# Kernel tuning notes

Measured on AMD Instinct MI355X. Metric: run time of the kernel, lower is better.

## Reference

```python
import jax, jax.numpy as jnp
import numpy as np
from jax import lax

B, CIN, COUT, H, W = 4, 256, 256, 64, 64
KH = KW = 3
K = KH * KW
GN_GROUPS = 32
EPS = 1e-5


def setup_inputs() -> dict:
    key = jax.random.key(0)
    ks = jax.random.split(key, 6)
    x = jax.random.normal(ks[0], (B, CIN, H, W), jnp.float32)
    # offset predictor conv: 3x3, 18 out channels, with bias (init small so offsets stay near 0)
    offset_w = jax.random.normal(ks[1], (2 * K, CIN, KH, KW), jnp.float32) * 0.01
    offset_b = jax.random.normal(ks[2], (2 * K,), jnp.float32) * 0.01
    # deformable conv weight (no bias), He-ish scale
    deform_w = jax.random.normal(ks[3], (COUT, CIN, KH, KW), jnp.float32) * (1.0 / np.sqrt(CIN * K))
    gn_gamma = jnp.ones((COUT,), jnp.float32)
    gn_beta = jnp.zeros((COUT,), jnp.float32)
    return {"x": x, "offset_w": offset_w, "offset_b": offset_b,
            "deform_w": deform_w, "gn_gamma": gn_gamma, "gn_beta": gn_beta}


def _deform_conv(x, offset, weight):
    """Deformable conv v1, stride=1, pad=1, dil=1, deformable_groups=1.
    x: [B,C,H,W]; offset: [B,2K,H,W] with (dy,dx) per kernel tap; weight: [O,C,3,3].
    """
    b, c, h, w = x.shape
    off = offset.reshape(b, K, 2, h, w)
    # base sampling grid per kernel tap: p = p0 - pad + k
    ky, kx = jnp.meshgrid(jnp.arange(KH), jnp.arange(KW), indexing="ij")
    base_y = (jnp.arange(h, dtype=jnp.float32) - 1.0)[None, :, None] + ky.reshape(K).astype(jnp.float32)[:, None, None]  # [K,H,1]
    base_x = (jnp.arange(w, dtype=jnp.float32) - 1.0)[None, None, :] + kx.reshape(K).astype(jnp.float32)[:, None, None]  # [K,1,W]
    py = base_y[None] + off[:, :, 0]  # [B,K,H,W]
    px = base_x[None] + off[:, :, 1]  # [B,K,H,W]

    y0 = jnp.floor(py)
    x0 = jnp.floor(px)
    ty = py - y0
    tx = px - x0
    y0 = y0.astype(jnp.int32)
    x0 = x0.astype(jnp.int32)

    x_hw = x.transpose(0, 2, 3, 1).reshape(b, h * w, c)  # [B,HW,C]

    def corner(yi, xi, wgt):
        valid = (yi >= 0) & (yi < h) & (xi >= 0) & (xi < w)
        yc = jnp.clip(yi, 0, h - 1)
        xc = jnp.clip(xi, 0, w - 1)
        idx = (yc * w + xc).reshape(b, K * h * w)
        v = jnp.take_along_axis(x_hw, idx[..., None], axis=1)  # [B,KHW,C]
        return v * (wgt * valid.astype(wgt.dtype)).reshape(b, K * h * w, 1)

    samp = (corner(y0, x0, (1 - ty) * (1 - tx))
            + corner(y0, x0 + 1, (1 - ty) * tx)
            + corner(y0 + 1, x0, ty * (1 - tx))
            + corner(y0 + 1, x0 + 1, ty * tx))  # [B,KHW,C]
    samp = samp.reshape(b, K, h, w, c)
    return jnp.einsum("bkhwc,ock->bohw", samp, weight.reshape(weight.shape[0], c, K))


def reference(x, offset_w, offset_b, deform_w, gn_gamma, gn_beta):
    # offset = conv3x3(x) + bias
    offset = lax.conv_general_dilated(
        x, offset_w, window_strides=(1, 1), padding=((1, 1), (1, 1)),
        dimension_numbers=("NCHW", "OIHW", "NCHW")) + offset_b[None, :, None, None]
    out = _deform_conv(x, offset, deform_w)
    # GroupNorm(32, COUT) + ReLU
    b, c, h, w = out.shape
    g = out.reshape(b, GN_GROUPS, (c // GN_GROUPS) * h * w)
    mu = g.mean(axis=2, keepdims=True)
    var = g.var(axis=2, keepdims=True)
    g = (g - mu) * lax.rsqrt(var + EPS)
    out = g.reshape(b, c, h, w) * gn_gamma[None, :, None, None] + gn_beta[None, :, None, None]
    return jax.nn.relu(out)
```

## Files before the change

### kernel.cpp

```cpp
#include <hip/hip_runtime.h>
#include <hip/hip_bf16.h>
#include <stdint.h>


typedef unsigned short u16;
typedef __bf16 bf16x8 __attribute__((ext_vector_type(8)));
typedef float f32x4_t __attribute__((ext_vector_type(4)));

#define HW 4096

__device__ __forceinline__ uint32_t f32_to_bf16_rne(float f) {
  uint32_t u = __builtin_bit_cast(uint32_t, f);
  return (u + 0x7FFFu + ((u >> 16) & 1u)) >> 16;
}
__device__ __forceinline__ float bf_lo(uint32_t u) {
  return __builtin_bit_cast(float, u << 16);
}
__device__ __forceinline__ float bf_hi(uint32_t u) {
  return __builtin_bit_cast(float, u & 0xFFFF0000u);
}

__global__ __launch_bounds__(256) void k_transpose(const float* __restrict__ x,
                                                   u16* __restrict__ xt) {
  __shared__ float tile[32][33];
  int b = blockIdx.z;
  int c0 = blockIdx.y * 32;
  int p0 = blockIdx.x * 32;
  int tx = threadIdx.x, ty = threadIdx.y;
#pragma unroll
  for (int j = 0; j < 32; j += 8)
    tile[ty + j][tx] = x[(b * 256 + c0 + ty + j) * HW + p0 + tx];
  __syncthreads();
  int wid = ty * 32 + tx;
  int cp = wid & 15;
  int pr = wid >> 4;
#pragma unroll
  for (int j = 0; j < 2; j++) {
    int p = pr + j * 16;
    uint32_t lo = f32_to_bf16_rne(tile[cp * 2][p]);
    uint32_t hi = f32_to_bf16_rne(tile[cp * 2 + 1][p]);
    *(uint32_t*)&xt[(b * HW + p0 + p) * 256 + c0 + cp * 2] = lo | (hi << 16);
  }
}

__global__ __launch_bounds__(256) void k_prep_w(const float* __restrict__ wsrc,
                                                u16* __restrict__ warr) {
  int e = blockIdx.x * 256 + threadIdx.x;
  int kk = e & 7, m = (e >> 3) & 255, g = (e >> 11) & 7, kc = e >> 14;
  int cin = (kc & 3) * 64 + g * 8 + kk;
  int tap = kc >> 2;
  float v = wsrc[m * 2304 + cin * 9 + tap];
  warr[e] = (u16)f32_to_bf16_rne(v);
}

__global__ __launch_bounds__(256) void k_prep_owm(const float* __restrict__ ow,
                                                  u16* __restrict__ owm) {
  int e = blockIdx.x * 256 + threadIdx.x;
  int kk = e & 7, m = (e >> 3) & 31, g = (e >> 8) & 7, kc = e >> 11;
  int cin = (kc & 3) * 64 + g * 8 + kk;
  int tap = kc >> 2;
  float v = (m < 18) ? ow[m * 2304 + cin * 9 + tap] : 0.f;
  owm[e] = (u16)f32_to_bf16_rne(v);
}

__global__ __launch_bounds__(256) void k_conv(
    const u16* __restrict__ xt, const u16* __restrict__ warr,
    const u16* __restrict__ owm, const float* __restrict__ ob,
    float* __restrict__ out) {
  __shared__ char smem[27136];
  u16* stage = (u16*)smem;
  float* off_part = (float*)(smem + 16896);
  int4* ci_s = (int4*)smem;
  float4* mw_s = (float4*)(smem + 4608);
  u16* b_s = (u16*)(smem + 16896);

  int tid = threadIdx.x;
  int lane = tid & 63;
  int wm = tid >> 6;
  int b = blockIdx.x >> 7;
  int pt = blockIdx.x & 127;
  int p0 = pt * 32;
  int yrow = p0 >> 6, xbase = p0 & 63;

  {
    u16* st = stage + wm * 2112;
    int q = lane & 15, pq = lane >> 4;
    f32x4_t a2[2][2] = {};
#pragma unroll 1
    for (int tap = wm; tap < 9; tap += 4) {
      int ky = tap / 3, kx = tap % 3;
      int yy = yrow + ky - 1;
      bool vy = (yy >= 0) && (yy < 64);
#pragma unroll
      for (int cc = 0; cc < 4; cc++) {
        int kc = tap * 4 + cc;
#pragma unroll
        for (int i = 0; i < 8; i++) {
          int px = i * 4 + pq;
          int xx2 = xbase + px + kx - 1;
          uint2 v = make_uint2(0u, 0u);
          if (vy && xx2 >= 0 && xx2 < 64)
            v = *(const uint2*)&xt[(b * HW + yy * 64 + xx2) * 256 + cc * 64 + q * 4];
          *(uint2*)&st[(q >> 1) * 264 + px * 8 + (q & 1) * 4] = v;
        }
#pragma unroll
        for (int ks = 0; ks < 2; ks++) {
          int g = ks * 4 + pq;
          const u16* ab = owm + kc * 2048 + g * 256;
#pragma unroll
          for (int s = 0; s < 2; s++) {
            bf16x8 bfr = *(bf16x8*)&st[g * 264 + (s * 16 + q) * 8];
#pragma unroll
            for (int im = 0; im < 2; im++) {
              bf16x8 af = *(const bf16x8*)&ab[(im * 16 + q) * 8];
              a2[s][im] = __builtin_amdgcn_mfma_f32_16x16x32_bf16(af, bfr, a2[s][im], 0, 0, 0);
            }
          }
        }
      }
    }
#pragma unroll
    for (int s = 0; s < 2; s++)
#pragma unroll
      for (int im = 0; im < 2; im++)
#pragma unroll
        for (int r = 0; r < 4; r++) {
          int oc = im * 16 + pq * 4 + r;
          if (oc < 18) off_part[(wm * 32 + s * 16 + q) * 20 + oc] = a2[s][im][r];
        }
  }
  __syncthreads();
  for (int it = tid; it < 288; it += 256) {
    int tap = it >> 5;
    int px = it & 31;
    float dy = ob[2 * tap], dx = ob[2 * tap + 1];
#pragma unroll
    for (int wv = 0; wv < 4; wv++) {
      dy += off_part[(wv * 32 + px) * 20 + 2 * tap];
      dx += off_part[(wv * 32 + px) * 20 + 2 * tap + 1];
    }
    int ky = tap / 3, kx = tap % 3;
    int p = p0 + px;
    int yq = p >> 6, xq = p & 63;
    float py = (float)(yq - 1 + ky) + dy;
    float pxx = (float)(xq - 1 + kx) + dx;
    float y0f = floorf(py), x0f = floorf(pxx);
    float ty = py - y0f, tx = pxx - x0f;
    int y0 = (int)y0f, x0 = (int)x0f;
    int y1 = y0 + 1, x1 = x0 + 1;
    float wy0 = 1.f - ty, wy1 = ty, wx0 = 1.f - tx, wx1 = tx;
    bool vy0 = (y0 >= 0) && (y0 < 64), vy1 = (y1 >= 0) && (y1 < 64);
    bool vx0 = (x0 >= 0) && (x0 < 64), vx1 = (x1 >= 0) && (x1 < 64);
    int cy0 = min(max(y0, 0), 63), cy1 = min(max(y1, 0), 63);
    int cx0 = min(max(x0, 0), 63), cx1 = min(max(x1, 0), 63);
    int base = b * HW;
    int4 ci;
    ci.x = (base + cy0 * 64 + cx0) * 256;
    ci.y = (base + cy0 * 64 + cx1) * 256;
    ci.z = (base + cy1 * 64 + cx0) * 256;
    ci.w = (base + cy1 * 64 + cx1) * 256;
    float4 mw;
    mw.x = wy0 * wx0 * ((vy0 && vx0) ? 1.f : 0.f);
    mw.y = wy0 * wx1 * ((vy0 && vx1) ? 1.f : 0.f);
    mw.z = wy1 * wx0 * ((vy1 && vx0) ? 1.f : 0.f);
    mw.w = wy1 * wx1 * ((vy1 && vx1) ? 1.f : 0.f);
    ci_s[it] = ci;
    mw_s[it] = mw;
  }
  __syncthreads();

  int q = tid & 15, pxb = (tid >> 4) & 15;
  f32x4_t acc[2][4] = {};
#pragma unroll 1
  for (int tap = 0; tap < 9; tap++) {
    int4 ci0 = ci_s[tap * 32 + pxb];
    int4 ci1 = ci_s[tap * 32 + 16 + pxb];
    float4 mw0 = mw_s[tap * 32 + pxb];
    float4 mw1 = mw_s[tap * 32 + 16 + pxb];
#pragma unroll
    for (int cc = 0; cc < 4; cc++) {
      int kc = tap * 4 + cc;
      int e = cc * 64 + q * 4;
      u16* bb = b_s + (kc & 1) * 2176;
      {
        uint2 c0v = *(const uint2*)&xt[ci0.x + e];
        uint2 c1v = *(const uint2*)&xt[ci0.y + e];
        uint2 c2v = *(const uint2*)&xt[ci0.z + e];
        uint2 c3v = *(const uint2*)&xt[ci0.w + e];
        float r0 = mw0.x * bf_lo(c0v.x) + mw0.y * bf_lo(c1v.x) + mw0.z * bf_lo(c2v.x) + mw0.w * bf_lo(c3v.x);
        float r1 = mw0.x * bf_hi(c0v.x) + mw0.y * bf_hi(c1v.x) + mw0.z * bf_hi(c2v.x) + mw0.w * bf_hi(c3v.x);
        float r2 = mw0.x * bf_lo(c0v.y) + mw0.y * bf_lo(c1v.y) + mw0.z * bf_lo(c2v.y) + mw0.w * bf_lo(c3v.y);
        float r3 = mw0.x * bf_hi(c0v.y) + mw0.y * bf_hi(c1v.y) + mw0.z * bf_hi(c2v.y) + mw0.w * bf_hi(c3v.y);
        uint2 u;
        u.x = f32_to_bf16_rne(r0) | (f32_to_bf16_rne(r1) << 16);
        u.y = f32_to_bf16_rne(r2) | (f32_to_bf16_rne(r3) << 16);
        *(uint2*)&bb[(q >> 1) * 136 + pxb * 8 + (q & 1) * 4] = u;
      }
      {
        uint2 c0v = *(const uint2*)&xt[ci1.x + e];
        uint2 c1v = *(const uint2*)&xt[ci1.y + e];
        uint2 c2v = *(const uint2*)&xt[ci1.z + e];
        uint2 c3v = *(const uint2*)&xt[ci1.w + e];
        float r0 = mw1.x * bf_lo(c0v.x) + mw1.y * bf_lo(c1v.x) + mw1.z * bf_lo(c2v.x) + mw1.w * bf_lo(c3v.x);
        float r1 = mw1.x * bf_hi(c0v.x) + mw1.y * bf_hi(c1v.x) + mw1.z * bf_hi(c2v.x) + mw1.w * bf_hi(c3v.x);
        float r2 = mw1.x * bf_lo(c0v.y) + mw1.y * bf_lo(c1v.y) + mw1.z * bf_lo(c2v.y) + mw1.w * bf_lo(c3v.y);
        float r3 = mw1.x * bf_hi(c0v.y) + mw1.y * bf_hi(c1v.y) + mw1.z * bf_hi(c2v.y) + mw1.w * bf_hi(c3v.y);
        uint2 u;
        u.x = f32_to_bf16_rne(r0) | (f32_to_bf16_rne(r1) << 16);
        u.y = f32_to_bf16_rne(r2) | (f32_to_bf16_rne(r3) << 16);
        *(uint2*)&bb[1088 + (q >> 1) * 136 + pxb * 8 + (q & 1) * 4] = u;
      }
      __syncthreads();
#pragma unroll
      for (int ks = 0; ks < 2; ks++) {
        int g = ks * 4 + (lane >> 4);
        bf16x8 b0 = *(bf16x8*)&bb[g * 136 + (lane & 15) * 8];
        bf16x8 b1 = *(bf16x8*)&bb[1088 + g * 136 + (lane & 15) * 8];
        const u16* ab = warr + kc * 16384 + g * 2048 + (wm * 64 + (lane & 15)) * 8;
#pragma unroll
        for (int im = 0; im < 4; im++) {
          bf16x8 af = *(const bf16x8*)&ab[im * 128];
          acc[0][im] = __builtin_amdgcn_mfma_f32_16x16x32_bf16(af, b0, acc[0][im], 0, 0, 0);
          acc[1][im] = __builtin_amdgcn_mfma_f32_16x16x32_bf16(af, b1, acc[1][im], 0, 0, 0);
        }
      }
    }
  }
  int rq = lane >> 4;
#pragma unroll
  for (int s = 0; s < 2; s++) {
    int n = p0 + s * 16 + (lane & 15);
#pragma unroll
    for (int im = 0; im < 4; im++)
#pragma unroll
      for (int r = 0; r < 4; r++) {
        int m = wm * 64 + im * 16 + rq * 4 + r;
        out[(b * 256 + m) * HW + n] = acc[s][im][r];
      }
  }
}

__global__ __launch_bounds__(256) void k_gn_part(const float* __restrict__ out,
                                                 float2* __restrict__ part) {
  int blk = blockIdx.x;
  int bg = blk >> 2, qt = blk & 3;
  const float4* base = (const float4*)(out + (size_t)bg * 32768 + (size_t)qt * 8192);
  int tid = threadIdx.x;
  float s = 0.f, ss = 0.f;
#pragma unroll
  for (int i = 0; i < 8; i++) {
    float4 v = base[tid + i * 256];
    s += v.x + v.y + v.z + v.w;
    ss += v.x * v.x + v.y * v.y + v.z * v.z + v.w * v.w;
  }
#pragma unroll
  for (int m = 1; m < 64; m <<= 1) {
    s += __shfl_xor(s, m);
    ss += __shfl_xor(ss, m);
  }
  __shared__ float ls[4], lss[4];
  int wv = tid >> 6, lane = tid & 63;
  if (lane == 0) { ls[wv] = s; lss[wv] = ss; }
  __syncthreads();
  if (tid == 0)
    part[blk] = make_float2(ls[0] + ls[1] + ls[2] + ls[3],
                            lss[0] + lss[1] + lss[2] + lss[3]);
}

__global__ __launch_bounds__(256) void k_gn_apply(float* __restrict__ out,
                                                  const float2* __restrict__ part,
                                                  const float* __restrict__ gamma,
                                                  const float* __restrict__ beta) {
  __shared__ float sga, sbe;
  int gid = blockIdx.x * 256 + threadIdx.x;
  int c = (gid >> 10) & 255;
  int bb = gid >> 18;
  if (threadIdx.x == 0) {
    int p4 = (bb * 32 + (c >> 3)) * 4;
    float s = 0.f, ss = 0.f;
#pragma unroll
    for (int j = 0; j < 4; j++) {
      float2 p = part[p4 + j];
      s += p.x;
      ss += p.y;
    }
    float mu = s / 32768.f;
    float var = ss / 32768.f - mu * mu;
    float rs = rsqrtf(var + 1e-5f);
    float ga = gamma[c] * rs;
    sga = ga;
    sbe = beta[c] - mu * ga;
  }
  __syncthreads();
  float ga = sga, be = sbe;
  float4 v = ((const float4*)out)[gid];
  v.x = fmaxf(v.x * ga + be, 0.f);
  v.y = fmaxf(v.y * ga + be, 0.f);
  v.z = fmaxf(v.z * ga + be, 0.f);
  v.w = fmaxf(v.w * ga + be, 0.f);
  ((float4*)out)[gid] = v;
}

extern "C" void kernel_launch(void* const* d_in, const int* in_sizes, int n_in,
                              void* d_out, int out_size, void* d_ws, size_t ws_size,
                              hipStream_t stream) {
  const float* x = (const float*)d_in[0];
  const float* offset_w = (const float*)d_in[1];
  const float* offset_b = (const float*)d_in[2];
  const float* deform_w = (const float*)d_in[3];
  const float* gn_gamma = (const float*)d_in[4];
  const float* gn_beta = (const float*)d_in[5];
  float* out = (float*)d_out;
  char* ws = (char*)d_ws;

  u16* xt = (u16*)ws;
  u16* warr = (u16*)(ws + 8388608);
  u16* owm = (u16*)(ws + 9568256);
  float2* part = (float2*)(ws + 9715712);

  k_transpose<<<dim3(128, 8, 4), dim3(32, 8), 0, stream>>>(x, xt);
  k_prep_w<<<dim3(2304), dim3(256), 0, stream>>>(deform_w, warr);
  k_prep_owm<<<dim3(288), dim3(256), 0, stream>>>(offset_w, owm);
  k_conv<<<dim3(512), dim3(256), 0, stream>>>(xt, warr, owm, offset_b, out);
  k_gn_part<<<dim3(512), dim3(256), 0, stream>>>(out, part);
  k_gn_apply<<<dim3(4096), dim3(256), 0, stream>>>(out, part, gn_gamma, gn_beta);
}
```

Measured before the change: 173.6 us.

## Fuse GN stats into deform conv, widen to 512 threads, merge prep kernels

Merges the two weight-prep kernels into one launch that also zeroes the GroupNorm partial buffer. The deformable conv kernel moves to 512 threads with 8 waves, each owning 32 output channels. It uses 16-byte gathers, prefetches the next chunk's bilinear corner loads before the MFMA work, and processes 128 channels per barrier instead of 64. GroupNorm sum and sum-of-squares are now reduced in the conv epilogue and accumulated with atomics, which removes the separate stats pass over the output, at the cost of atomic contention and more LDS per block.

Result: faster. 163.4 us (-5.9%).

```diff
diff --git a/kernel.cpp b/kernel.cpp
--- a/kernel.cpp
+++ b/kernel.cpp
@@ -18,6 +18,12 @@
 }
 __device__ __forceinline__ float bf_hi(uint32_t u) {
   return __builtin_bit_cast(float, u & 0xFFFF0000u);
+}
+__device__ __forceinline__ uint32_t blend2(uint32_t a, uint32_t b, uint32_t c,
+                                           uint32_t d, float4 mw) {
+  float lo = mw.x * bf_lo(a) + mw.y * bf_lo(b) + mw.z * bf_lo(c) + mw.w * bf_lo(d);
+  float hi = mw.x * bf_hi(a) + mw.y * bf_hi(b) + mw.z * bf_hi(c) + mw.w * bf_hi(d);
+  return f32_to_bf16_rne(lo) | (f32_to_bf16_rne(hi) << 16);
 }
 
 __global__ __launch_bounds__(256) void k_transpose(const float* __restrict__ x,
@@ -43,36 +49,40 @@
   }
 }
 
-__global__ __launch_bounds__(256) void k_prep_w(const float* __restrict__ wsrc,
-                                                u16* __restrict__ warr) {
-  int e = blockIdx.x * 256 + threadIdx.x;
-  int kk = e & 7, m = (e >> 3) & 255, g = (e >> 11) & 7, kc = e >> 14;
-  int cin = (kc & 3) * 64 + g * 8 + kk;
-  int tap = kc >> 2;
-  float v = wsrc[m * 2304 + cin * 9 + tap];
-  warr[e] = (u16)f32_to_bf16_rne(v);
-}
-
-__global__ __launch_bounds__(256) void k_prep_owm(const float* __restrict__ ow,
-                                                  u16* __restrict__ owm) {
-  int e = blockIdx.x * 256 + threadIdx.x;
-  int kk = e & 7, m = (e >> 3) & 31, g = (e >> 8) & 7, kc = e >> 11;
-  int cin = (kc & 3) * 64 + g * 8 + kk;
-  int tap = kc >> 2;
-  float v = (m < 18) ? ow[m * 2304 + cin * 9 + tap] : 0.f;
-  owm[e] = (u16)f32_to_bf16_rne(v);
-}
-
-__global__ __launch_bounds__(256) void k_conv(
+__global__ __launch_bounds__(256) void k_prep(const float* __restrict__ wsrc,
+                                              const float* __restrict__ ow,
+                                              u16* __restrict__ warr,
+                                              u16* __restrict__ owm,
+                                              float* __restrict__ part) {
+  int bid = blockIdx.x;
+  if (bid < 2304) {
+    int e = bid * 256 + threadIdx.x;
+    int kk = e & 7, m = (e >> 3) & 255, g = (e >> 11) & 7, kc = e >> 14;
+    int cin = (kc & 3) * 64 + g * 8 + kk;
+    int tap = kc >> 2;
+    warr[e] = (u16)f32_to_bf16_rne(wsrc[m * 2304 + cin * 9 + tap]);
+  } else if (bid < 2592) {
+    int e = (bid - 2304) * 256 + threadIdx.x;
+    int kk = e & 7, m = (e >> 3) & 31, g = (e >> 8) & 7, kc = e >> 11;
+    int cin = (kc & 3) * 64 + g * 8 + kk;
+    int tap = kc >> 2;
+    float v = (m < 18) ? ow[m * 2304 + cin * 9 + tap] : 0.f;
+    owm[e] = (u16)f32_to_bf16_rne(v);
+  } else {
+    part[threadIdx.x] = 0.f;
+  }
+}
+
+__global__ __launch_bounds__(512, 4) void k_conv(
     const u16* __restrict__ xt, const u16* __restrict__ warr,
     const u16* __restrict__ owm, const float* __restrict__ ob,
-    float* __restrict__ out) {
-  __shared__ char smem[27136];
+    float* __restrict__ out, float* __restrict__ part) {
+  __shared__ char smem[54272];
   u16* stage = (u16*)smem;
-  float* off_part = (float*)(smem + 16896);
+  float* off_part = (float*)(smem + 33792);
   int4* ci_s = (int4*)smem;
   float4* mw_s = (float4*)(smem + 4608);
-  u16* b_s = (u16*)(smem + 16896);
+  u16* b_s = (u16*)(smem + 9216);
 
   int tid = threadIdx.x;
   int lane = tid & 63;
@@ -85,36 +95,34 @@
   {
     u16* st = stage + wm * 2112;
     int q = lane & 15, pq = lane >> 4;
+    int oct = lane & 7, pxs = lane >> 3;
     f32x4_t a2[2][2] = {};
 #pragma unroll 1
-    for (int tap = wm; tap < 9; tap += 4) {
+    for (int kc = wm; kc < 36; kc += 8) {
+      int tap = kc >> 2, cc = kc & 3;
       int ky = tap / 3, kx = tap % 3;
       int yy = yrow + ky - 1;
       bool vy = (yy >= 0) && (yy < 64);
 #pragma unroll
-      for (int cc = 0; cc < 4; cc++) {
-        int kc = tap * 4 + cc;
-#pragma unroll
-        for (int i = 0; i < 8; i++) {
-          int px = i * 4 + pq;
-          int xx2 = xbase + px + kx - 1;
-          uint2 v = make_uint2(0u, 0u);
-          if (vy && xx2 >= 0 && xx2 < 64)
-            v = *(const uint2*)&xt[(b * HW + yy * 64 + xx2) * 256 + cc * 64 + q * 4];
-          *(uint2*)&st[(q >> 1) * 264 + px * 8 + (q & 1) * 4] = v;
-        }
-#pragma unroll
-        for (int ks = 0; ks < 2; ks++) {
-          int g = ks * 4 + pq;
-          const u16* ab = owm + kc * 2048 + g * 256;
-#pragma unroll
-          for (int s = 0; s < 2; s++) {
-            bf16x8 bfr = *(bf16x8*)&st[g * 264 + (s * 16 + q) * 8];
-#pragma unroll
-            for (int im = 0; im < 2; im++) {
-              bf16x8 af = *(const bf16x8*)&ab[(im * 16 + q) * 8];
-              a2[s][im] = __builtin_amdgcn_mfma_f32_16x16x32_bf16(af, bfr, a2[s][im], 0, 0, 0);
-            }
+      for (int i = 0; i < 4; i++) {
+        int px = i * 8 + pxs;
+        int xx2 = xbase + px + kx - 1;
+        uint4 v = make_uint4(0u, 0u, 0u, 0u);
+        if (vy && xx2 >= 0 && xx2 < 64)
+          v = *(const uint4*)&xt[(b * HW + yy * 64 + xx2) * 256 + cc * 64 + oct * 8];
+        *(uint4*)&st[oct * 264 + px * 8] = v;
+      }
+#pragma unroll
+      for (int ks = 0; ks < 2; ks++) {
+        int g = ks * 4 + pq;
+        const u16* ab = owm + kc * 2048 + g * 256;
+#pragma unroll
+        for (int s = 0; s < 2; s++) {
+          bf16x8 bfr = *(bf16x8*)&st[g * 264 + (s * 16 + q) * 8];
+#pragma unroll
+          for (int im = 0; im < 2; im++) {
+            bf16x8 af = *(const bf16x8*)&ab[(im * 16 + q) * 8];
+            a2[s][im] = __builtin_amdgcn_mfma_f32_16x16x32_bf16(af, bfr, a2[s][im], 0, 0, 0);
           }
         }
       }
@@ -130,12 +138,12 @@
         }
   }
   __syncthreads();
-  for (int it = tid; it < 288; it += 256) {
+  for (int it = tid; it < 288; it += 512) {
     int tap = it >> 5;
     int px = it & 31;
     float dy = ob[2 * tap], dx = ob[2 * tap + 1];
 #pragma unroll
-    for (int wv = 0; wv < 4; wv++) {
+    for (int wv = 0; wv < 8; wv++) {
       dy += off_part[(wv * 32 + px) * 20 + 2 * tap];
       dx += off_part[(wv * 32 + px) * 20 + 2 * tap + 1];
     }
@@ -169,102 +177,91 @@
   }
   __syncthreads();
 
-  int q = tid & 15, pxb = (tid >> 4) & 15;
-  f32x4_t acc[2][4] = {};
+  {
+    int oct8 = tid & 15;
+    int pxg = tid >> 4;
+    int sub = pxg >> 4;
+    int pxw = pxg & 15;
+    int col = lane & 15;
+    int pq = lane >> 4;
+    f32x4_t acc[2][2] = {};
+
+    int4 ci = ci_s[pxg];
+    float4 mw = mw_s[pxg];
+    int e = oct8 * 8;
+    uint4 c0 = *(const uint4*)&xt[ci.x + e];
+    uint4 c1 = *(const uint4*)&xt[ci.y + e];
+    uint4 c2 = *(const uint4*)&xt[ci.z + e];
+    uint4 c3 = *(const uint4*)&xt[ci.w + e];
+
 #pragma unroll 1
-  for (int tap = 0; tap < 9; tap++) {
-    int4 ci0 = ci_s[tap * 32 + pxb];
-    int4 ci1 = ci_s[tap * 32 + 16 + pxb];
-    float4 mw0 = mw_s[tap * 32 + pxb];
-    float4 mw1 = mw_s[tap * 32 + 16 + pxb];
-#pragma unroll
-    for (int cc = 0; cc < 4; cc++) {
-      int kc = tap * 4 + cc;
-      int e = cc * 64 + q * 4;
-      u16* bb = b_s + (kc & 1) * 2176;
-      {
-        uint2 c0v = *(const uint2*)&xt[ci0.x + e];
-        uint2 c1v = *(const uint2*)&xt[ci0.y + e];
-        uint2 c2v = *(const uint2*)&xt[ci0.z + e];
-        uint2 c3v = *(const uint2*)&xt[ci0.w + e];
-        float r0 = mw0.x * bf_lo(c0v.x) + mw0.y * bf_lo(c1v.x) + mw0.z * bf_lo(c2v.x) + mw0.w * bf_lo(c3v.x);
-        float r1 = mw0.x * bf_hi(c0v.x) + mw0.y * bf_hi(c1v.x) + mw0.z * bf_hi(c2v.x) + mw0.w * bf_hi(c3v.x);
-        float r2 = mw0.x * bf_lo(c0v.y) + mw0.y * bf_lo(c1v.y) + mw0.z * bf_lo(c2v.y) + mw0.w * bf_lo(c3v.y);
-        float r3 = mw0.x * bf_hi(c0v.y) + mw0.y * bf_hi(c1v.y) + mw0.z * bf_hi(c2v.y) + mw0.w * bf_hi(c3v.y);
-        uint2 u;
-        u.x = f32_to_bf16_rne(r0) | (f32_to_bf16_rne(r1) << 16);
-        u.y = f32_to_bf16_rne(r2) | (f32_to_bf16_rne(r3) << 16);
-        *(uint2*)&bb[(q >> 1) * 136 + pxb * 8 + (q & 1) * 4] = u;
-      }
-      {
-        uint2 c0v = *(const uint2*)&xt[ci1.x + e];
-        uint2 c1v = *(const uint2*)&xt[ci1.y + e];
-        uint2 c2v = *(const uint2*)&xt[ci1.z + e];
-        uint2 c3v = *(const uint2*)&xt[ci1.w + e];
-        float r0 = mw1.x * bf_lo(c0v.x) + mw1.y * bf_lo(c1v.x) + mw1.z * bf_lo(c2v.x) + mw1.w * bf_lo(c3v.x);
-        float r1 = mw1.x * bf_hi(c0v.x) + mw1.y * bf_hi(c1v.x) + mw1.z * bf_hi(c2v.x) + mw1.w * bf_hi(c3v.x);
-        float r2 = mw1.x * bf_lo(c0v.y) + mw1.y * bf_lo(c1v.y) + mw1.z * bf_lo(c2v.y) + mw1.w * bf_lo(c3v.y);
-        float r3 = mw1.x * bf_hi(c0v.y) + mw1.y * bf_hi(c1v.y) + mw1.z * bf_hi(c2v.y) + mw1.w * bf_hi(c3v.y);
-        uint2 u;
-        u.x = f32_to_bf16_rne(r0) | (f32_to_bf16_rne(r1) << 16);
-        u.y = f32_to_bf16_rne(r2) | (f32_to_bf16_rne(r3) << 16);
-        *(uint2*)&bb[1088 + (q >> 1) * 136 + pxb * 8 + (q & 1) * 4] = u;
-      }
+    for (int dccg = 0; dccg < 18; dccg++) {
+      u16* bb = b_s + (dccg & 1) * 4352;
+      uint4 u;
+      u.x = blend2(c0.x, c1.x, c2.x, c3.x, mw);
+      u.y = blend2(c0.y, c1.y, c2.y, c3.y, mw);
+      u.z = blend2(c0.z, c1.z, c2.z, c3.z, mw);
+      u.w = blend2(c0.w, c1.w, c2.w, c3.w, mw);
+      *(uint4*)&bb[sub * 2176 + oct8 * 136 + pxw * 8] = u;
       __syncthreads();
-#pragma unroll
-      for (int ks = 0; ks < 2; ks++) {
-        int g = ks * 4 + (lane >> 4);
-        bf16x8 b0 = *(bf16x8*)&bb[g * 136 + (lane & 15) * 8];
-        bf16x8 b1 = *(bf16x8*)&bb[1088 + g * 136 + (lane & 15) * 8];
-        const u16* ab = warr + kc * 16384 + g * 2048 + (wm * 64 + (lane & 15)) * 8;
-#pragma unroll
-        for (int im = 0; im < 4; im++) {
+      if (dccg < 17) {
+        int nx = dccg + 1;
+        int tapn = nx >> 1;
+        int en = (nx & 1) * 128 + oct8 * 8;
+        int4 cin = ci_s[tapn * 32 + pxg];
+        float4 mwn = mw_s[tapn * 32 + pxg];
+        c0 = *(const uint4*)&xt[cin.x + en];
+        c1 = *(const uint4*)&xt[cin.y + en];
+        c2 = *(const uint4*)&xt[cin.z + en];
+        c3 = *(const uint4*)&xt[cin.w + en];
+        mw = mwn;
+      }
+      int tap = dccg >> 1, dcc = dccg & 1;
+#pragma unroll
+      for (int ks = 0; ks < 4; ks++) {
+        int ro = ks * 4 + pq;
+        bf16x8 b0 = *(bf16x8*)&bb[ro * 136 + col * 8];
+        bf16x8 b1 = *(bf16x8*)&bb[2176 + ro * 136 + col * 8];
+        int kc = tap * 4 + dcc * 2 + (ks >> 1);
+        int g = (ks & 1) * 4 + pq;
+        const u16* ab = warr + kc * 16384 + g * 2048 + (wm * 32 + col) * 8;
+#pragma unroll
+        for (int im = 0; im < 2; im++) {
           bf16x8 af = *(const bf16x8*)&ab[im * 128];
           acc[0][im] = __builtin_amdgcn_mfma_f32_16x16x32_bf16(af, b0, acc[0][im], 0, 0, 0);
           acc[1][im] = __builtin_amdgcn_mfma_f32_16x16x32_bf16(af, b1, acc[1][im], 0, 0, 0);
         }
       }
     }
-  }
-  int rq = lane >> 4;
-#pragma unroll
-  for (int s = 0; s < 2; s++) {
-    int n = p0 + s * 16 + (lane & 15);
-#pragma unroll
-    for (int im = 0; im < 4; im++)
-#pragma unroll
-      for (int r = 0; r < 4; r++) {
-        int m = wm * 64 + im * 16 + rq * 4 + r;
-        out[(b * 256 + m) * HW + n] = acc[s][im][r];
-      }
-  }
-}
-
-__global__ __launch_bounds__(256) void k_gn_part(const float* __restrict__ out,
-                                                 float2* __restrict__ part) {
-  int blk = blockIdx.x;
-  int bg = blk >> 2, qt = blk & 3;
-  const float4* base = (const float4*)(out + (size_t)bg * 32768 + (size_t)qt * 8192);
-  int tid = threadIdx.x;
-  float s = 0.f, ss = 0.f;
-#pragma unroll
-  for (int i = 0; i < 8; i++) {
-    float4 v = base[tid + i * 256];
-    s += v.x + v.y + v.z + v.w;
-    ss += v.x * v.x + v.y * v.y + v.z * v.z + v.w * v.w;
-  }
-#pragma unroll
-  for (int m = 1; m < 64; m <<= 1) {
-    s += __shfl_xor(s, m);
-    ss += __shfl_xor(ss, m);
-  }
-  __shared__ float ls[4], lss[4];
-  int wv = tid >> 6, lane = tid & 63;
-  if (lane == 0) { ls[wv] = s; lss[wv] = ss; }
-  __syncthreads();
-  if (tid == 0)
-    part[blk] = make_float2(ls[0] + ls[1] + ls[2] + ls[3],
-                            lss[0] + lss[1] + lss[2] + lss[3]);
+
+#pragma unroll
+    for (int im = 0; im < 2; im++) {
+      float s = 0.f, ss = 0.f;
+#pragma unroll
+      for (int sb = 0; sb < 2; sb++) {
+        int n = p0 + sb * 16 + col;
+#pragma unroll
+        for (int r = 0; r < 4; r++) {
+          int m = wm * 32 + im * 16 + pq * 4 + r;
+          float v = acc[sb][im][r];
+          out[(b * 256 + m) * HW + n] = v;
+          s += v;
+          ss += v * v;
+        }
+      }
+#pragma unroll
+      for (int msk = 1; msk <= 16; msk <<= 1) {
+        s += __shfl_xor(s, msk);
+        ss += __shfl_xor(ss, msk);
+      }
+      if ((lane & 31) == 0) {
+        int g = wm * 4 + im * 2 + (lane >> 5);
+        float* pp = part + (b * 32 + g) * 2;
+        atomicAdd(pp, s);
+        atomicAdd(pp + 1, ss);
+      }
+    }
+  }
 }
 
 __global__ __launch_bounds__(256) void k_gn_apply(float* __restrict__ out,
@@ -276,16 +273,9 @@
   int c = (gid >> 10) & 255;
   int bb = gid >> 18;
   if (threadIdx.x == 0) {
-    int p4 = (bb * 32 + (c >> 3)) * 4;
-    float s = 0.f, ss = 0.f;
-#pragma unroll
-    for (int j = 0; j < 4; j++) {
-      float2 p = part[p4 + j];
-      s += p.x;
-      ss += p.y;
-    }
-    float mu = s / 32768.f;
-    float var = ss / 32768.f - mu * mu;
+    float2 p = part[bb * 32 + (c >> 3)];
+    float mu = p.x / 32768.f;
+    float var = p.y / 32768.f - mu * mu;
     float rs = rsqrtf(var + 1e-5f);
     float ga = gamma[c] * rs;
     sga = ga;
@@ -316,12 +306,10 @@
   u16* xt = (u16*)ws;
   u16* warr = (u16*)(ws + 8388608);
   u16* owm = (u16*)(ws + 9568256);
-  float2* part = (float2*)(ws + 9715712);
+  float* part = (float*)(ws + 9715712);
 
   k_transpose<<<dim3(128, 8, 4), dim3(32, 8), 0, stream>>>(x, xt);
-  k_prep_w<<<dim3(2304), dim3(256), 0, stream>>>(deform_w, warr);
-  k_prep_owm<<<dim3(288), dim3(256), 0, stream>>>(offset_w, owm);
-  k_conv<<<dim3(512), dim3(256), 0, stream>>>(xt, warr, owm, offset_b, out);
-  k_gn_part<<<dim3(512), dim3(256), 0, stream>>>(out, part);
-  k_gn_apply<<<dim3(4096), dim3(256), 0, stream>>>(out, part, gn_gamma, gn_beta);
-}
+  k_prep<<<dim3(2593), dim3(256), 0, stream>>>(deform_w, offset_w, warr, owm, part);
+  k_conv<<<dim3(512), dim3(512), 0, stream>>>(xt, warr, owm, offset_b, out, part);
+  k_gn_apply<<<dim3(4096), dim3(256), 0, stream>>>(out, (const float2*)part, gn_gamma, gn_beta);
+}
```
